# Kernel optimization log

Hardware: AMD Instinct MI355X
Metric: run time of the kernel (lower is better)

The kernel has to match this reference:

```python
import jax, jax.numpy as jnp
import numpy as np

B, CQ, CKV, H, W = 8, 256, 512, 64, 64
HKV, WKV = 32, 32
DQK = CQ // 8  # 32


def setup_inputs() -> dict:
    key = jax.random.key(0)
    ks = jax.random.split(key, 9)
    s = 0.05
    return {
        "query": jax.random.normal(ks[0], (B, CQ, H, W), jnp.float32),
        "key_value": jax.random.normal(ks[1], (B, CKV, HKV, WKV), jnp.float32),
        "Wq": jax.random.normal(ks[2], (DQK, CQ), jnp.float32) * s,
        "bq": jax.random.normal(ks[3], (DQK,), jnp.float32) * s,
        "Wk": jax.random.normal(ks[4], (DQK, CKV), jnp.float32) * s,
        "bk": jax.random.normal(ks[5], (DQK,), jnp.float32) * s,
        "Wv": jax.random.normal(ks[6], (CQ, CKV), jnp.float32) * s,
        "bv": jax.random.normal(ks[7], (CQ,), jnp.float32) * s,
        "gamma": jax.random.normal(ks[8], (1,), jnp.float32) * 0.5,
    }


def reference(query, key_value, Wq, bq, Wk, bk, Wv, bv, gamma):
    b, cq, h, w = query.shape
    n = h * w
    # bilinear resize of key_value to query's spatial size (align_corners=False
    # half-pixel convention, matching torch F.interpolate and jax.image.resize)
    kv = jax.image.resize(key_value, (b, key_value.shape[1], h, w), method="bilinear")
    # 1x1 convs are channel contractions
    q = jnp.einsum("bchw,dc->bdhw", query, Wq) + bq[None, :, None, None]   # [B,DQK,H,W]
    k = jnp.einsum("bchw,dc->bdhw", kv, Wk) + bk[None, :, None, None]      # [B,DQK,H,W]
    v = jnp.einsum("bchw,dc->bdhw", kv, Wv) + bv[None, :, None, None]      # [B,CQ,H,W]
    qf = q.reshape(b, -1, n)   # [B,DQK,N]
    kf = k.reshape(b, -1, n)   # [B,DQK,N]
    vf = v.reshape(b, -1, n)   # [B,CQ,N]
    energy = jnp.einsum("bdn,bdm->bnm", qf, kf)        # [B,N,N]
    attention = jax.nn.softmax(energy, axis=-1)
    out = jnp.einsum("bnm,bcm->bcn", attention, vf)     # [B,CQ,N]
    out = out.reshape(b, cq, h, w)
    return gamma[0] * out + query
```

## Files before the change

kernel.cpp:

```cpp
#include <hip/hip_runtime.h>

#define B_ 8
#define CQ_ 256
#define CKV_ 512
#define N_ 4096
#define DQK_ 32

typedef __bf16 bf16;
typedef __bf16 bf16x4 __attribute__((ext_vector_type(4)));
typedef __bf16 bf16x8 __attribute__((ext_vector_type(8)));
typedef float f32x4 __attribute__((ext_vector_type(4)));

__global__ void k_convert_w(const float* __restrict__ Wq, const float* __restrict__ Wk,
                            const float* __restrict__ Wv,
                            bf16* __restrict__ wq, bf16* __restrict__ wk, bf16* __restrict__ wv) {
    int i = blockIdx.x * 256 + threadIdx.x;
    if (i < 8192) wq[i] = (bf16)Wq[i];
    else if (i < 24576) wk[i - 8192] = (bf16)Wk[i - 8192];
    else if (i < 155648) wv[i - 24576] = (bf16)Wv[i - 24576];
}

__global__ __launch_bounds__(256) void k_resize(const float* __restrict__ kv, bf16* __restrict__ kvr) {
    const int yo = blockIdx.x;
    const int b  = blockIdx.y;
    const int tid = threadIdx.x;
    __shared__ float r0[64][33];
    __shared__ float r1[64][33];
    int ty = yo >> 1;
    int y0, y1; float wy0, wy1;
    if ((yo & 1) == 0) { y0 = ty > 0 ? ty - 1 : 0; y1 = ty; wy0 = 0.25f; wy1 = 0.75f; }
    else               { y0 = ty; y1 = ty < 31 ? ty + 1 : 31; wy0 = 0.75f; wy1 = 0.25f; }
    const int u_loc = tid & 63;
    const int xo_base = tid >> 6;
    for (int uc = 0; uc < CKV_; uc += 64) {
        __syncthreads();
        for (int i = 0; i < 8; ++i) {
            int idx = tid + i * 256;
            int u = idx >> 5, x = idx & 31;
            const float* src = kv + ((size_t)b * CKV_ + uc + u) * 1024 + x;
            r0[u][x] = src[y0 * 32];
            r1[u][x] = src[y1 * 32];
        }
        __syncthreads();
        for (int i = 0; i < 16; ++i) {
            int xo = xo_base + i * 4;
            int tx = xo >> 1;
            int xa, xb; float wxa, wxb;
            if ((xo & 1) == 0) { xa = tx > 0 ? tx - 1 : 0; xb = tx; wxa = 0.25f; wxb = 0.75f; }
            else               { xa = tx; xb = tx < 31 ? tx + 1 : 31; wxa = 0.75f; wxb = 0.25f; }
            float v0 = wxa * r0[u_loc][xa] + wxb * r0[u_loc][xb];
            float v1 = wxa * r1[u_loc][xa] + wxb * r1[u_loc][xb];
            float val = wy0 * v0 + wy1 * v1;
            kvr[((size_t)b * N_ + yo * 64 + xo) * CKV_ + uc + u_loc] = (bf16)val;
        }
    }
}

__global__ __launch_bounds__(256) void k_proj_q_fused(const float* __restrict__ query,
                                                      const bf16* __restrict__ W,
                                                      const float* __restrict__ bias,
                                                      bf16* __restrict__ qTb) {
    __shared__ bf16 tile[64][264];
    const int n0 = blockIdx.x * 64;
    const int b  = blockIdx.y;
    const int tid = threadIdx.x;
    const int xi = tid & 15, c0 = tid >> 4;
    for (int pass = 0; pass < 16; ++pass) {
        int c = c0 + pass * 16;
        const float4 v = *(const float4*)(query + ((size_t)b * CQ_ + c) * N_ + n0 + xi * 4);
        tile[xi * 4 + 0][c] = (bf16)v.x;
        tile[xi * 4 + 1][c] = (bf16)v.y;
        tile[xi * 4 + 2][c] = (bf16)v.z;
        tile[xi * 4 + 3][c] = (bf16)v.w;
    }
    __syncthreads();
    const int w = tid >> 6, lane = tid & 63;
    const int l16 = lane & 15, quad = lane >> 4;
    const int ct = w & 1, nh = w >> 1;
    f32x4 acc[2];
    acc[0] = (f32x4){0.f, 0.f, 0.f, 0.f}; acc[1] = (f32x4){0.f, 0.f, 0.f, 0.f};
    const bf16* aptr = W + (ct * 16 + l16) * CQ_ + quad * 8;
#pragma unroll
    for (int ks = 0; ks < 8; ++ks) {
        bf16x8 af = *(const bf16x8*)(aptr + ks * 32);
        for (int j = 0; j < 2; ++j) {
            bf16x8 bfv = *(const bf16x8*)&tile[nh * 32 + j * 16 + l16][ks * 32 + quad * 8];
            acc[j] = __builtin_amdgcn_mfma_f32_16x16x32_bf16(af, bfv, acc[j], 0, 0, 0);
        }
    }
    const float LOG2E = 1.4426950408889634f;
    for (int j = 0; j < 2; ++j)
        for (int r = 0; r < 4; ++r) {
            int d = ct * 16 + quad * 4 + r;
            int n = n0 + nh * 32 + j * 16 + l16;
            qTb[((size_t)b * N_ + n) * DQK_ + d] = (bf16)((acc[j][r] + bias[d]) * LOG2E);
        }
}

__global__ __launch_bounds__(256) void k_proj_k(const bf16* __restrict__ W,
                                                const float* __restrict__ bias,
                                                const bf16* __restrict__ Bm,
                                                bf16* __restrict__ outT) {
    const int mb = blockIdx.x * 128;
    const int b  = blockIdx.y;
    const int tid = threadIdx.x;
    const int w = tid >> 6, lane = tid & 63;
    const int l16 = lane & 15, quad = lane >> 4;
    const int ct = w & 1;
    const int mhalf = (w >> 1) * 64;
    f32x4 acc[4];
    for (int j = 0; j < 4; ++j) acc[j] = (f32x4){0.f, 0.f, 0.f, 0.f};
    const bf16* aptr  = W + (ct * 16 + l16) * CKV_ + quad * 8;
    const bf16* bbase = Bm + ((size_t)b * N_ + mb + mhalf) * CKV_ + quad * 8;
#pragma unroll
    for (int ks = 0; ks < 16; ++ks) {
        bf16x8 af = *(const bf16x8*)(aptr + ks * 32);
        for (int j = 0; j < 4; ++j) {
            bf16x8 bfv = *(const bf16x8*)(bbase + (size_t)(j * 16 + l16) * CKV_ + ks * 32);
            acc[j] = __builtin_amdgcn_mfma_f32_16x16x32_bf16(af, bfv, acc[j], 0, 0, 0);
        }
    }
    for (int j = 0; j < 4; ++j)
        for (int r = 0; r < 4; ++r) {
            int d = ct * 16 + quad * 4 + r;
            int m = mb + mhalf + j * 16 + l16;
            outT[((size_t)b * N_ + m) * DQK_ + d] = (bf16)(acc[j][r] + bias[d]);
        }
}

__global__ __launch_bounds__(256) void k_proj_v(const bf16* __restrict__ W,
                                                const float* __restrict__ bias,
                                                const bf16* __restrict__ Bm,
                                                bf16* __restrict__ vout) {
    const int mb = blockIdx.x * 64;
    const int b  = blockIdx.y;
    const int tid = threadIdx.x;
    const int w = tid >> 6, lane = tid & 63;
    const int l16 = lane & 15, quad = lane >> 4;
    f32x4 acc[4][4];
    for (int i = 0; i < 4; ++i) for (int j = 0; j < 4; ++j) acc[i][j] = (f32x4){0.f, 0.f, 0.f, 0.f};
    const bf16* bbase = Bm + ((size_t)b * N_ + mb) * CKV_ + quad * 8;
#pragma unroll 4
    for (int ks = 0; ks < 16; ++ks) {
        bf16x8 bfv[4];
        for (int j = 0; j < 4; ++j)
            bfv[j] = *(const bf16x8*)(bbase + (size_t)(j * 16 + l16) * CKV_ + ks * 32);
        for (int i = 0; i < 4; ++i) {
            bf16x8 af = *(const bf16x8*)(W + (size_t)((w * 4 + i) * 16 + l16) * CKV_ + ks * 32 + quad * 8);
            for (int j = 0; j < 4; ++j)
                acc[i][j] = __builtin_amdgcn_mfma_f32_16x16x32_bf16(af, bfv[j], acc[i][j], 0, 0, 0);
        }
    }
    for (int i = 0; i < 4; ++i)
        for (int r = 0; r < 4; ++r) {
            int c = (w * 4 + i) * 16 + quad * 4 + r;
            float bvs = bias[c];
            for (int j = 0; j < 4; ++j) {
                int m = mb + j * 16 + l16;
                vout[((size_t)b * CQ_ + c) * N_ + m] = (bf16)(acc[i][j][r] + bvs);
            }
        }
}

__global__ __launch_bounds__(256, 2) void k_flash(const bf16* __restrict__ qT,
                                                  const bf16* __restrict__ kT,
                                                  const bf16* __restrict__ vv,
                                                  const float* __restrict__ query,
                                                  const float* __restrict__ gamma,
                                                  float* __restrict__ out) {
    __shared__ bf16 P[4][64][72];
    const int b  = blockIdx.x;
    const int n0 = blockIdx.y * 64;
    const int tid = threadIdx.x;
    const int w = tid >> 6, lane = tid & 63;
    const int l16 = lane & 15, quad = lane >> 4;
    const int swz = (l16 & 3) ^ ((l16 >> 3) << 1);

    bf16x8 qfrag[4];
    for (int jn = 0; jn < 4; ++jn)
        qfrag[jn] = *(const bf16x8*)(qT + ((size_t)b * N_ + n0 + jn * 16 + l16) * DQK_ + quad * 8);

    const bf16 one = (bf16)1.0f;
    const bf16x8 ones = {one, one, one, one, one, one, one, one};
    const f32x4 zed = {0.f, 0.f, 0.f, 0.f};

    f32x4 acc[4][4];
    for (int i = 0; i < 4; ++i) for (int j = 0; j < 4; ++j) acc[i][j] = zed;
    f32x4 accl[4];
    for (int j = 0; j < 4; ++j) accl[j] = zed;

    const bf16* kp = kT + ((size_t)b * N_ + l16) * DQK_ + quad * 8;
    const bf16* vp[4];
    for (int i = 0; i < 4; ++i)
        vp[i] = vv + ((size_t)b * CQ_ + w * 64 + i * 16 + l16) * N_ + quad * 8;

    bf16 (* __restrict__ Pw)[72] = P[w];

    bf16x8 kf[4], vf[2][4], pf[2][4];
    for (int im = 0; im < 4; ++im) kf[im] = *(const bf16x8*)(kp + im * 16 * DQK_);
    kp += 64 * DQK_;

    for (int mt = 0; mt < 64; ++mt) {
        if (mt)
            for (int ks = 0; ks < 2; ++ks)
                for (int j = 0; j < 4; ++j)
                    pf[ks][j] = *(const bf16x8*)&Pw[j * 16 + l16]
                                    [((((ks << 1) | (quad >> 1)) ^ swz) << 4) + ((quad & 1) << 3)];
        for (int jn = 0; jn < 4; ++jn)
            for (int im = 0; im < 4; ++im) {
                f32x4 s = __builtin_amdgcn_mfma_f32_16x16x32_bf16(kf[im], qfrag[jn], zed, 0, 0, 0);
                bf16x4 pk;
                for (int r = 0; r < 4; ++r) pk[r] = (bf16)__builtin_amdgcn_exp2f(s[r]);
                *(bf16x4*)&Pw[jn * 16 + l16][((im ^ swz) << 4) + quad * 4] = pk;
            }
        for (int im = 0; im < 4; ++im) kf[im] = *(const bf16x8*)(kp + im * 16 * DQK_);
        kp += 64 * DQK_;
        if (mt)
            for (int ks = 0; ks < 2; ++ks)
                for (int j = 0; j < 4; ++j) {
                    accl[j] = __builtin_amdgcn_mfma_f32_16x16x32_bf16(ones, pf[ks][j], accl[j], 0, 0, 0);
                    for (int i = 0; i < 4; ++i)
                        acc[i][j] = __builtin_amdgcn_mfma_f32_16x16x32_bf16(vf[ks][i], pf[ks][j], acc[i][j], 0, 0, 0);
                }
        for (int ks = 0; ks < 2; ++ks)
            for (int i = 0; i < 4; ++i)
                vf[ks][i] = *(const bf16x8*)(vp[i] + ks * 32);
        for (int i = 0; i < 4; ++i) vp[i] += 64;
    }
    for (int ks = 0; ks < 2; ++ks)
        for (int j = 0; j < 4; ++j)
            pf[ks][j] = *(const bf16x8*)&Pw[j * 16 + l16]
                            [((((ks << 1) | (quad >> 1)) ^ swz) << 4) + ((quad & 1) << 3)];
    for (int ks = 0; ks < 2; ++ks)
        for (int j = 0; j < 4; ++j) {
            accl[j] = __builtin_amdgcn_mfma_f32_16x16x32_bf16(ones, pf[ks][j], accl[j], 0, 0, 0);
            for (int i = 0; i < 4; ++i)
                acc[i][j] = __builtin_amdgcn_mfma_f32_16x16x32_bf16(vf[ks][i], pf[ks][j], acc[i][j], 0, 0, 0);
        }

    float linv[4];
    for (int j = 0; j < 4; ++j) linv[j] = 1.f / accl[j][0];
    const float g = gamma[0];
    for (int i = 0; i < 4; ++i)
        for (int r = 0; r < 4; ++r) {
            int c = w * 64 + i * 16 + quad * 4 + r;
            for (int j = 0; j < 4; ++j) {
                int n = n0 + j * 16 + l16;
                size_t idx = ((size_t)b * CQ_ + c) * N_ + n;
                out[idx] = g * acc[i][j][r] * linv[j] + query[idx];
            }
        }
}

extern "C" void kernel_launch(void* const* d_in, const int* in_sizes, int n_in,
                              void* d_out, int out_size, void* d_ws, size_t ws_size,
                              hipStream_t stream) {
    const float* query     = (const float*)d_in[0];
    const float* key_value = (const float*)d_in[1];
    const float* Wq = (const float*)d_in[2];
    const float* bq = (const float*)d_in[3];
    const float* Wk = (const float*)d_in[4];
    const float* bk = (const float*)d_in[5];
    const float* Wv = (const float*)d_in[6];
    const float* bv = (const float*)d_in[7];
    const float* gamma = (const float*)d_in[8];
    float* out = (float*)d_out;

    char* ws = (char*)d_ws;
    bf16* kvr  = (bf16*)(ws);
    bf16* vbuf = (bf16*)(ws + 33554432);
    bf16* qTb  = (bf16*)(ws + 50331648);
    bf16* kTb  = (bf16*)(ws + 52428800);
    bf16* wqb  = (bf16*)(ws + 54525952);
    bf16* wkb  = (bf16*)(ws + 54542336);
    bf16* wvb  = (bf16*)(ws + 54575104);

    k_convert_w<<<608, 256, 0, stream>>>(Wq, Wk, Wv, wqb, wkb, wvb);
    k_resize<<<dim3(64, 8), 256, 0, stream>>>(key_value, kvr);
    k_proj_q_fused<<<dim3(64, 8), 256, 0, stream>>>(query, wqb, bq, qTb);
    k_proj_k<<<dim3(32, 8), 256, 0, stream>>>(wkb, bk, kvr, kTb);
    k_proj_v<<<dim3(64, 8), 256, 0, stream>>>(wvb, bv, kvr, vbuf);
    k_flash<<<dim3(8, 64), 256, 0, stream>>>(qTb, kTb, vbuf, query, gamma, out);
}
```

Before: 345.6 us.

## Share P tile across warps instead of recomputing QK^T exp per warp

Each warp previously computed the full 64x64 exp(QK^T) tile redundantly, once per warp, for its own channel slice. Now each warp computes only its 16 query rows and writes them into a shared double-buffered P tile. All warps then read the whole tile after a block-wide barrier. This removes 4x redundant score MFMAs and exp work per tile and halves LDS use, but adds a __syncthreads every iteration and drops the register prefetch of V and K across iterations.

```diff
diff --git a/kernel.cpp b/kernel.cpp
--- a/kernel.cpp
+++ b/kernel.cpp
@@ -168,7 +168,7 @@
                                                   const float* __restrict__ query,
                                                   const float* __restrict__ gamma,
                                                   float* __restrict__ out) {
-    __shared__ bf16 P[4][64][72];
+    __shared__ bf16 P[2][64][72];
     const int b  = blockIdx.x;
     const int n0 = blockIdx.y * 64;
     const int tid = threadIdx.x;
@@ -176,9 +176,7 @@
     const int l16 = lane & 15, quad = lane >> 4;
     const int swz = (l16 & 3) ^ ((l16 >> 3) << 1);
 
-    bf16x8 qfrag[4];
-    for (int jn = 0; jn < 4; ++jn)
-        qfrag[jn] = *(const bf16x8*)(qT + ((size_t)b * N_ + n0 + jn * 16 + l16) * DQK_ + quad * 8);
+    bf16x8 qfrag = *(const bf16x8*)(qT + ((size_t)b * N_ + n0 + w * 16 + l16) * DQK_ + quad * 8);
 
     const bf16 one = (bf16)1.0f;
     const bf16x8 ones = {one, one, one, one, one, one, one, one};
@@ -189,54 +187,48 @@
     f32x4 accl[4];
     for (int j = 0; j < 4; ++j) accl[j] = zed;
 
-    const bf16* kp = kT + ((size_t)b * N_ + l16) * DQK_ + quad * 8;
-    const bf16* vp[4];
-    for (int i = 0; i < 4; ++i)
-        vp[i] = vv + ((size_t)b * CQ_ + w * 64 + i * 16 + l16) * N_ + quad * 8;
-
-    bf16 (* __restrict__ Pw)[72] = P[w];
-
-    bf16x8 kf[4], vf[2][4], pf[2][4];
-    for (int im = 0; im < 4; ++im) kf[im] = *(const bf16x8*)(kp + im * 16 * DQK_);
-    kp += 64 * DQK_;
+    const bf16* kbase = kT + (size_t)b * N_ * DQK_;
+    const bf16* vbase = vv + ((size_t)b * CQ_ + w * 64) * N_;
+
+    for (int im = 0; im < 4; ++im) {
+        bf16x8 kf = *(const bf16x8*)(kbase + (size_t)(im * 16 + l16) * DQK_ + quad * 8);
+        f32x4 s = __builtin_amdgcn_mfma_f32_16x16x32_bf16(kf, qfrag, zed, 0, 0, 0);
+        bf16x4 pk;
+        for (int r = 0; r < 4; ++r) pk[r] = (bf16)__builtin_amdgcn_exp2f(s[r]);
+        *(bf16x4*)&P[0][w * 16 + l16][((im ^ swz) << 4) + quad * 4] = pk;
+    }
 
     for (int mt = 0; mt < 64; ++mt) {
-        if (mt)
-            for (int ks = 0; ks < 2; ++ks)
-                for (int j = 0; j < 4; ++j)
-                    pf[ks][j] = *(const bf16x8*)&Pw[j * 16 + l16]
-                                    [((((ks << 1) | (quad >> 1)) ^ swz) << 4) + ((quad & 1) << 3)];
-        for (int jn = 0; jn < 4; ++jn)
+        __syncthreads();
+        const int m0 = mt * 64;
+        bf16 (* __restrict__ Pb)[72] = P[mt & 1];
+        bf16x8 pf[2][4];
+        for (int ks = 0; ks < 2; ++ks)
+            for (int j = 0; j < 4; ++j)
+                pf[ks][j] = *(const bf16x8*)&Pb[j * 16 + l16]
+                                [((((ks << 1) | (quad >> 1)) ^ swz) << 4) + ((quad & 1) << 3)];
+        bf16x8 vf[2][4];
+        for (int ks = 0; ks < 2; ++ks)
+            for (int i = 0; i < 4; ++i)
+                vf[ks][i] = *(const bf16x8*)(vbase + (size_t)(i * 16 + l16) * N_ + m0 + ks * 32 + quad * 8);
+        if (mt < 63) {
+            const int m1 = m0 + 64;
+            bf16 (* __restrict__ Pn)[72] = P[(mt + 1) & 1];
             for (int im = 0; im < 4; ++im) {
-                f32x4 s = __builtin_amdgcn_mfma_f32_16x16x32_bf16(kf[im], qfrag[jn], zed, 0, 0, 0);
+                bf16x8 kf = *(const bf16x8*)(kbase + (size_t)(m1 + im * 16 + l16) * DQK_ + quad * 8);
+                f32x4 s = __builtin_amdgcn_mfma_f32_16x16x32_bf16(kf, qfrag, zed, 0, 0, 0);
                 bf16x4 pk;
                 for (int r = 0; r < 4; ++r) pk[r] = (bf16)__builtin_amdgcn_exp2f(s[r]);
-                *(bf16x4*)&Pw[jn * 16 + l16][((im ^ swz) << 4) + quad * 4] = pk;
-            }
-        for (int im = 0; im < 4; ++im) kf[im] = *(const bf16x8*)(kp + im * 16 * DQK_);
-        kp += 64 * DQK_;
-        if (mt)
-            for (int ks = 0; ks < 2; ++ks)
-                for (int j = 0; j < 4; ++j) {
-                    accl[j] = __builtin_amdgcn_mfma_f32_16x16x32_bf16(ones, pf[ks][j], accl[j], 0, 0, 0);
-                    for (int i = 0; i < 4; ++i)
-                        acc[i][j] = __builtin_amdgcn_mfma_f32_16x16x32_bf16(vf[ks][i], pf[ks][j], acc[i][j], 0, 0, 0);
-                }
+                *(bf16x4*)&Pn[w * 16 + l16][((im ^ swz) << 4) + quad * 4] = pk;
+            }
+        }
         for (int ks = 0; ks < 2; ++ks)
-            for (int i = 0; i < 4; ++i)
-                vf[ks][i] = *(const bf16x8*)(vp[i] + ks * 32);
-        for (int i = 0; i < 4; ++i) vp[i] += 64;
-    }
-    for (int ks = 0; ks < 2; ++ks)
-        for (int j = 0; j < 4; ++j)
-            pf[ks][j] = *(const bf16x8*)&Pw[j * 16 + l16]
-                            [((((ks << 1) | (quad >> 1)) ^ swz) << 4) + ((quad & 1) << 3)];
-    for (int ks = 0; ks < 2; ++ks)
-        for (int j = 0; j < 4; ++j) {
-            accl[j] = __builtin_amdgcn_mfma_f32_16x16x32_bf16(ones, pf[ks][j], accl[j], 0, 0, 0);
-            for (int i = 0; i < 4; ++i)
-                acc[i][j] = __builtin_amdgcn_mfma_f32_16x16x32_bf16(vf[ks][i], pf[ks][j], acc[i][j], 0, 0, 0);
-        }
+            for (int j = 0; j < 4; ++j) {
+                accl[j] = __builtin_amdgcn_mfma_f32_16x16x32_bf16(ones, pf[ks][j], accl[j], 0, 0, 0);
+                for (int i = 0; i < 4; ++i)
+                    acc[i][j] = __builtin_amdgcn_mfma_f32_16x16x32_bf16(vf[ks][i], pf[ks][j], acc[i][j], 0, 0, 0);
+            }
+    }
 
     float linv[4];
     for (int j = 0; j < 4; ++j) linv[j] = 1.f / accl[j][0];
```

New measurement: 355.2 us. 2.8% more time.
